# Optimization experiments

Measured on AMD Instinct MI355X. Metric: run time of the kernel, lower is better.

## Reference

```python
import jax, jax.numpy as jnp
import numpy as np

C_IN = 96          # spectral bands
D2 = 2 * C_IN      # d = 192 (inner dim)
D4 = 4 * D2        # 768 (4-directional scan channels)
N = 16             # SSM state size
DR = 6             # delta_rank = ceil(96/16)
B, H, W = 2, 96, 96  # H,W not in {8,16,32,64} -> s=1 path


def setup_inputs() -> dict:
    key = jax.random.key(0)
    ks = jax.random.split(key, 8)
    g = lambda k, shape, s: jax.random.normal(k, shape, jnp.float32) * s
    return {
        "x": jax.random.normal(ks[0], (B, C_IN, H, W), jnp.float32),
        "W_in": g(ks[1], (C_IN, 2 * D2), 0.05),          # in_proj (in,out)
        "b_in": jnp.zeros((2 * D2,), jnp.float32),
        "w_dw": g(ks[2], (D2, 1, 3, 3), 0.1),            # depthwise conv OIHW
        "b_dw": jnp.zeros((D2,), jnp.float32),
        "A_log": jnp.log(jnp.tile(jnp.arange(1.0, N + 1.0, dtype=jnp.float32), (D4, 1))),
        "Dp": jnp.ones((D4,), jnp.float32),
        "W_x": g(ks[3], (D4, DR + 2 * N), 0.05),         # x_proj, no bias
        "W_delta": g(ks[4], (DR, D4), 0.1),
        "b_delta": g(ks[5], (D4,), 0.1),
        "ln_g": jnp.ones((D2,), jnp.float32),
        "ln_b": jnp.zeros((D2,), jnp.float32),
        "W_out": g(ks[6], (D2, C_IN), 0.05),             # out_proj, no bias
    }


def _selective_scan(u, delta, A, Bm, Cm, Dv):
    # u, delta: [b,L,d4]; Bm, Cm: [b,L,n]; A: [d4,n]; Dv: [d4]
    b, L, d4 = u.shape
    n = A.shape[1]

    def step(h, inps):
        u_t, dt, B_t, C_t = inps                      # [b,d4],[b,d4],[b,n],[b,n]
        dA = jnp.exp(dt[:, :, None] * A)              # [b,d4,n]
        h = dA * h + (dt * u_t)[:, :, None] * B_t[:, None, :]
        y = jnp.einsum('bdn,bn->bd', h, C_t) + Dv * u_t
        return h, y

    h0 = jnp.zeros((b, d4, n), u.dtype)
    xs = (jnp.swapaxes(u, 0, 1), jnp.swapaxes(delta, 0, 1),
          jnp.swapaxes(Bm, 0, 1), jnp.swapaxes(Cm, 0, 1))
    _, ys = jax.lax.scan(step, h0, xs)                # ys: [L,b,d4]
    return jnp.swapaxes(ys, 0, 1)                     # [b,L,d4]


def reference(x, W_in, b_in, w_dw, b_dw, A_log, Dp, W_x, W_delta, b_delta, ln_g, ln_b, W_out):
    b, c, Hh, Ww = x.shape                            # s = 1 (H not in {8,16,32,64})
    d = W_in.shape[1] // 2
    # in_proj on channel-last, chunk into x / gate z
    xz = jnp.einsum('bchw,ce->bhwe', x, W_in) + b_in  # [b,h,w,2d]
    xx, z = jnp.split(xz, 2, axis=-1)
    # depthwise conv + silu
    xc = jnp.transpose(xx, (0, 3, 1, 2))              # [b,d,h,w]
    xc = jax.lax.conv_general_dilated(
        xc, w_dw, (1, 1), 'SAME', feature_group_count=d,
        dimension_numbers=('NCHW', 'OIHW', 'NCHW')) + b_dw[None, :, None, None]
    xc = jax.nn.silu(xc)
    # 4 directional flattenings (with s=1: x1==x2 row-major, x3==x4 reversed)
    L = Hh * Ww
    flat = xc.reshape(b, d, L)
    flipped = xc[:, :, ::-1, ::-1].reshape(b, d, L)
    xl = jnp.swapaxes(jnp.concatenate([flat, flat, flipped, flipped], axis=1), 1, 2)  # [b,L,4d]
    # SSM parameterization
    A = -jnp.exp(A_log)                               # [4d,n]
    x_dbl = xl @ W_x                                  # [b,L,dr+2n]
    dr, n = W_delta.shape[0], A.shape[1]
    dt_r = x_dbl[..., :dr]
    Bm = x_dbl[..., dr:dr + n]
    Cm = x_dbl[..., dr + n:]
    delta = jax.nn.softplus(dt_r @ W_delta + b_delta)  # [b,L,4d]
    y = _selective_scan(xl, delta, A, Bm, Cm, Dp)      # [b,L,4d]
    # merge 4 directions back to spatial
    y = jnp.transpose(y.reshape(b, L, 4, d), (0, 2, 3, 1))  # [b,4,d,L]
    y1 = y[:, 0].reshape(b, d, Hh, Ww)
    y2 = y[:, 1].reshape(b, d, Hh, Ww)
    y3 = y[:, 2].reshape(b, d, Hh, Ww)[:, :, ::-1, ::-1]
    y4 = y[:, 3].reshape(b, d, Hh, Ww)[:, :, ::-1, ::-1]
    yh = jnp.transpose(y1 + y2 + y3 + y4, (0, 2, 3, 1))  # [b,h,w,d]
    # LayerNorm over d
    mu = yh.mean(-1, keepdims=True)
    var = ((yh - mu) ** 2).mean(-1, keepdims=True)
    yn = (yh - mu) * jax.lax.rsqrt(var + 1e-5) * ln_g + ln_b
    out = (yn * jax.nn.silu(z)) @ W_out               # [b,h,w,c]
    return jnp.transpose(out, (0, 3, 1, 2))           # [b,c,h,w]
```

## Files before the change

### kernel.cpp

```cpp
#include <hip/hip_runtime.h>
#include <hip/hip_bf16.h>
#include <math.h>

#define CIN 96
#define D2 192
#define D4 768
#define LL 9216
#define NN 16
#define NCH 288
#define CLEN 32

typedef float v2f __attribute__((ext_vector_type(2)));

#define SZ_Y4SLOT (2u*2u*9216u*192u)
#define SZ_BL    (2u*9216u*192u)
#define SZ_XDBL  (2u*9216u*38u)
#define SZ_S     (2u*4u*288u*192u)
#define SZ_HSLOT (2u*4u*288u*192u*8u)
#define F_Y4     0u
#define F_XX     0u
#define F_ZS     (F_Y4 + SZ_Y4SLOT)
#define F_XT     (F_ZS + SZ_BL)
#define F_XD0    (F_XT + SZ_BL)
#define F_XD1    (F_XD0 + SZ_XDBL)
#define F_XD2    (F_XD1 + SZ_XDBL)
#define F_XD3    (F_XD2 + SZ_XDBL)
#define F_SBUF   (F_XD3 + SZ_XDBL)
#define F_HBUF   (F_SBUF + SZ_S)
#define F_WCOMB  (F_HBUF + SZ_HSLOT)
#define F_A0     (F_WCOMB + 15360u)
#define F_FF     (F_A0 + 768u)
#define F_XM     (F_FF + 768u)

__device__ __forceinline__ float silu_f(float z) {
    return z / (1.0f + __expf(-z));
}

__global__ __launch_bounds__(256) void k0_foldw(
    const float* __restrict__ Wx, const float* __restrict__ Alog,
    float* __restrict__ wcomb, float* __restrict__ A0f, float* __restrict__ Ffl)
{
    int i = blockIdx.x * 256 + threadIdx.x;
    if (i < 768) {
        float a0 = -__expf(Alog[i * 16]);
        bool fast = true;
        for (int n = 1; n < 16; n++) {
            float an = -__expf(Alog[i * 16 + n]);
            float tgt = (n + 1) * a0;
            fast = fast && (fabsf(an - tgt) <= 1e-5f * fabsf(tgt));
        }
        A0f[i] = a0;
        Ffl[i] = fast ? 1.f : 0.f;
    }
    if (i >= 192 * 80) return;
    int d = i / 80, j = i % 80;
    float v = 0.f;
    if (j < 38) v = Wx[d * 38 + j] + Wx[(d + 192) * 38 + j];
    else if (j >= 40 && j < 78) {
        int jj = j - 40;
        v = Wx[(d + 384) * 38 + jj] + Wx[(d + 576) * 38 + jj];
    }
    wcomb[i] = v;
}

__global__ __launch_bounds__(256) void k1_inproj(
    const float* __restrict__ x, const float* __restrict__ Win,
    const float* __restrict__ bin, float* __restrict__ xx,
    __hip_bfloat16* __restrict__ zs)
{
    __shared__ float xs[32][68];
    __shared__ float wsh[32][100];
    int tid = threadIdx.x;
    int bid = blockIdx.x;
    int eq = bid & 3;
    int lt = (bid >> 2) % 144;
    int b = bid / 576;
    int l0 = lt * 64;
    int e0 = eq * 96;

    int lg = tid & 15;
    int cg = tid >> 4;
    v2f acc[4][3];
#pragma unroll
    for (int i = 0; i < 4; i++)
#pragma unroll
        for (int p = 0; p < 3; p++) { acc[i][p].x = 0.f; acc[i][p].y = 0.f; }

    for (int kc = 0; kc < 96; kc += 32) {
        __syncthreads();
        for (int i = tid; i < 512; i += 256) {
            int kk = i >> 4, q = i & 15;
            float4 v = *(const float4*)&x[(size_t)(b * 96 + kc + kk) * LL + l0 + q * 4];
            *(float4*)&xs[kk][q * 4] = v;
        }
        for (int i = tid; i < 768; i += 256) {
            int kk = i / 24, q = i - kk * 24;
            float4 v = *(const float4*)&Win[(kc + kk) * 384 + e0 + q * 4];
            *(float4*)&wsh[kk][q * 4] = v;
        }
        __syncthreads();
#pragma unroll 4
        for (int k = 0; k < 32; k++) {
            float4 xv = *(const float4*)&xs[k][lg * 4];
            const v2f* wp = (const v2f*)&wsh[k][cg * 6];
            v2f w0 = wp[0], w1 = wp[1], w2 = wp[2];
            float xa[4] = {xv.x, xv.y, xv.z, xv.w};
#pragma unroll
            for (int i = 0; i < 4; i++) {
                v2f xi; xi.x = xa[i]; xi.y = xa[i];
                acc[i][0] += xi * w0;
                acc[i][1] += xi * w1;
                acc[i][2] += xi * w2;
            }
        }
    }
    if (eq < 2) {
#pragma unroll
        for (int j = 0; j < 6; j++) {
            int e = e0 + cg * 6 + j;
            float bb = bin[e];
            float4 v = {acc[0][j >> 1][j & 1] + bb, acc[1][j >> 1][j & 1] + bb,
                        acc[2][j >> 1][j & 1] + bb, acc[3][j >> 1][j & 1] + bb};
            *(float4*)&xx[(size_t)(b * 192 + e) * LL + l0 + lg * 4] = v;
        }
    } else {
        int zc0 = e0 - 192 + cg * 6;
        float bb[6];
#pragma unroll
        for (int j = 0; j < 6; j++) bb[j] = bin[e0 + cg * 6 + j];
#pragma unroll
        for (int i = 0; i < 4; i++) {
            int l = l0 + lg * 4 + i;
            __hip_bfloat16* zp = &zs[((size_t)b * LL + l) * 192 + zc0];
#pragma unroll
            for (int p = 0; p < 3; p++) {
                __hip_bfloat162 hv = __halves2bfloat162(
                    __float2bfloat16(silu_f(acc[i][p].x + bb[2 * p])),
                    __float2bfloat16(silu_f(acc[i][p].y + bb[2 * p + 1])));
                *(__hip_bfloat162*)&zp[2 * p] = hv;
            }
        }
    }
}

__global__ __launch_bounds__(192) void k2_conv(
    const float* __restrict__ xx, const float* __restrict__ wdw,
    const float* __restrict__ bdw, float* __restrict__ xt)
{
    __shared__ float tile[32][97];
    __shared__ float wsm[32][9];
    __shared__ float bs[32];
    int tid = threadIdx.x;
    int bid = blockIdx.x;
    int h = bid % 96;
    int r = bid / 96;
    int dg = r % 6;
    int b = r / 6;

    for (int i = tid; i < 288; i += 192) wsm[i / 9][i % 9] = wdw[(dg * 32 + i / 9) * 9 + (i % 9)];
    if (tid < 32) bs[tid] = bdw[dg * 32 + tid];
    __syncthreads();

    int w = tid % 96;
    int dhalf = tid / 96;
    for (int p = 0; p < 16; p++) {
        int dsub = 2 * p + dhalf;
        const float* base = xx + (size_t)(b * 192 + dg * 32 + dsub) * LL;
        float acc = bs[dsub];
#pragma unroll
        for (int kh = 0; kh < 3; kh++) {
            int hh = h + kh - 1;
            if (hh < 0 || hh >= 96) continue;
            const float* row = base + hh * 96;
#pragma unroll
            for (int kw = 0; kw < 3; kw++) {
                int ww = w + kw - 1;
                if (ww < 0 || ww >= 96) continue;
                acc += row[ww] * wsm[dsub][kh * 3 + kw];
            }
        }
        tile[dsub][w] = silu_f(acc);
    }
    __syncthreads();
    for (int i = tid; i < 768; i += 192) {
        int q = i & 7, ls = i >> 3;
        float4 v = {tile[q * 4 + 0][ls], tile[q * 4 + 1][ls], tile[q * 4 + 2][ls], tile[q * 4 + 3][ls]};
        *(float4*)&xt[((size_t)b * LL + h * 96 + ls) * 192 + dg * 32 + q * 4] = v;
    }
}

__global__ __launch_bounds__(320) void k3_xdbl(
    const float* __restrict__ xt, const float* __restrict__ wcomb,
    float* __restrict__ xa0, float* __restrict__ xa1,
    float* __restrict__ xb0, float* __restrict__ xb1)
{
    __shared__ float xs[16][68];
    __shared__ float wsh[16][80];
    int tid = threadIdx.x;
    int bid = blockIdx.x;
    int kh = bid & 1;
    int rt = (bid >> 1) % 144;
    int b = bid / 288;
    int r0 = rt * 64;
    int k0 = kh * 96;
    float* __restrict__ xa = kh ? xa1 : xa0;
    float* __restrict__ xb = kh ? xb1 : xb0;

    int rg = tid / 20;
    int cg = tid % 20;
    v2f acc[4][2];
#pragma unroll
    for (int i = 0; i < 4; i++)
#pragma unroll
        for (int p = 0; p < 2; p++) { acc[i][p].x = 0.f; acc[i][p].y = 0.f; }

    for (int kc = 0; kc < 96; kc += 16) {
        __syncthreads();
        if (tid < 256) {
            int row = tid >> 2, dq = tid & 3;
            float4 v = *(const float4*)&xt[((size_t)b * LL + r0 + row) * 192 + k0 + kc + dq * 4];
            xs[dq * 4 + 0][row] = v.x;
            xs[dq * 4 + 1][row] = v.y;
            xs[dq * 4 + 2][row] = v.z;
            xs[dq * 4 + 3][row] = v.w;
        }
        for (int i = tid; i < 16 * 80; i += 320) {
            int d = i / 80, j = i - d * 80;
            wsh[d][j] = wcomb[(k0 + kc + d) * 80 + j];
        }
        __syncthreads();
#pragma unroll
        for (int d = 0; d < 16; d++) {
            float4 xv = *(const float4*)&xs[d][rg * 4];
            float4 wv = *(const float4*)&wsh[d][cg * 4];
            v2f w01; w01.x = wv.x; w01.y = wv.y;
            v2f w23; w23.x = wv.z; w23.y = wv.w;
            float xr[4] = {xv.x, xv.y, xv.z, xv.w};
#pragma unroll
            for (int i = 0; i < 4; i++) {
                v2f xi; xi.x = xr[i]; xi.y = xr[i];
                acc[i][0] += xi * w01;
                acc[i][1] += xi * w23;
            }
        }
    }
    int c0 = cg * 4;
#pragma unroll
    for (int i = 0; i < 4; i++) {
        int la = r0 + rg * 4 + i;
#pragma unroll
        for (int j = 0; j < 4; j++) {
            int col = c0 + j;
            float v = acc[i][j >> 1][j & 1];
            if (col < 38) {
                xa[((size_t)b * LL + la) * 38 + col] = v;
            } else if (col >= 40 && col < 78) {
                int lb = LL - 1 - la;
                xb[((size_t)b * LL + lb) * 38 + (col - 40)] = v;
            }
        }
    }
}

__global__ __launch_bounds__(256) void k3s_merge(
    const float* __restrict__ a0, const float* __restrict__ a1,
    const float* __restrict__ b0, const float* __restrict__ b1,
    float* __restrict__ xm)
{
    int i = blockIdx.x * 256 + threadIdx.x;
    if (i < 2 * LL * 38) xm[i] = (a0[i] + a1[i]) + (b0[i] + b1[i]);
}

__global__ __launch_bounds__(192, 4) void k4_pass1(
    const float* __restrict__ xt, const float* __restrict__ xm,
    const float* __restrict__ Wd, const float* __restrict__ bdl,
    const float* __restrict__ Alog, const float* __restrict__ A0f,
    const float* __restrict__ Ffl,
    float* __restrict__ Sbuf, __hip_bfloat16* __restrict__ Hbuf)
{
    __shared__ float Bt[CLEN][16];
    __shared__ float Dt[CLEN][6];
    int tid = threadIdx.x;
    int bid = blockIdx.x;
    int k = bid % NCH;
    int r = bid / NCH;
    int dir = r & 3;
    int b = r >> 2;
    int l0 = k * CLEN;
    {
        const float* src = xm + ((size_t)b * LL + l0) * 38;
        for (int i = tid; i < CLEN * 38; i += 192) {
            int t = i / 38, j = i - t * 38;
            float v = src[i];
            if (j < 6) Dt[t][j] = v;
            else if (j < 22) Bt[t][j - 6] = v;
        }
    }
    __syncthreads();
    int c = tid;
    int d4 = dir * 192 + c;
    float a0 = A0f[d4];
    bool fast = (Ffl[d4] != 0.f);
    float wd[6];
#pragma unroll
    for (int rr = 0; rr < 6; rr++) wd[rr] = Wd[rr * 768 + d4];
    float bde = bdl[d4];
    float S = 0.f;
    int start = (dir < 2) ? l0 : (LL - 1 - l0);
    ptrdiff_t stp = (dir < 2) ? 192 : -192;
    const float* up = xt + (size_t)b * LL * 192 + (size_t)start * 192 + c;
    int bd = b * 4 + dir;
    size_t base = (((size_t)bd * NCH + k) * 192 + c) * 16;
    if (fast) {
        v2f h2[8];
#pragma unroll
        for (int n = 0; n < 8; n++) { h2[n].x = 0.f; h2[n].y = 0.f; }
#pragma unroll 2
        for (int t = 0; t < CLEN; t++) {
            float2 d01 = *(const float2*)&Dt[t][0];
            float2 d23 = *(const float2*)&Dt[t][2];
            float2 d45 = *(const float2*)&Dt[t][4];
            float s = bde + d01.x * wd[0] + d01.y * wd[1] + d23.x * wd[2]
                          + d23.y * wd[3] + d45.x * wd[4] + d45.y * wd[5];
            float dt = (s > 20.f) ? s : __logf(1.f + __expf(s));
            S += dt;
            float u = *up; up += stp;
            float du = dt * u;
            float e1 = __expf(dt * a0);
            float e2 = e1 * e1;
            v2f q; q.x = e1; q.y = e2;
            v2f e2v; e2v.x = e2; e2v.y = e2;
            v2f e4v = e2v * e2v;
            v2f q2 = q * e2v;
            v2f du2; du2.x = du; du2.y = du;
#pragma unroll
            for (int g = 0; g < 4; g++) {
                float4 bq = *(const float4*)&Bt[t][4 * g];
                v2f b0; b0.x = bq.x; b0.y = bq.y;
                v2f b1; b1.x = bq.z; b1.y = bq.w;
                h2[2 * g]     = q  * h2[2 * g]     + du2 * b0;
                h2[2 * g + 1] = q2 * h2[2 * g + 1] + du2 * b1;
                if (g < 3) { q *= e4v; q2 *= e4v; }
            }
        }
        __hip_bfloat16* hb = Hbuf + base;
#pragma unroll
        for (int n = 0; n < 8; n++) {
            hb[2 * n]     = __float2bfloat16(h2[n].x);
            hb[2 * n + 1] = __float2bfloat16(h2[n].y);
        }
    } else {
        float h[16];
#pragma unroll
        for (int n = 0; n < 16; n++) h[n] = 0.f;
        for (int t = 0; t < CLEN; t++) {
            float s = bde;
#pragma unroll
            for (int rr = 0; rr < 6; rr++) s += Dt[t][rr] * wd[rr];
            float dt = (s > 20.f) ? s : __logf(1.f + __expf(s));
            S += dt;
            float u = *up; up += stp;
            float du = dt * u;
#pragma unroll
            for (int n = 0; n < 16; n++) {
                float e = __expf(dt * (-__expf(Alog[d4 * 16 + n])));
                h[n] = e * h[n] + du * Bt[t][n];
            }
        }
#pragma unroll
        for (int n = 0; n < 16; n++) Hbuf[base + n] = __float2bfloat16(h[n]);
    }
    Sbuf[((size_t)bd * NCH + k) * 192 + c] = S;
}

__global__ __launch_bounds__(256) void k4_pass2(
    const float* __restrict__ Sbuf, const float* __restrict__ Alog,
    __hip_bfloat16* __restrict__ Hbuf)
{
    int lane = blockIdx.x * 256 + threadIdx.x;
    int bd = lane / 3072;
    int cn = lane % 3072;
    int c = cn >> 4, n = cn & 15;
    int dir = bd & 3;
    float an = -__expf(Alog[(dir * 192 + c) * 16 + n]);
    float h = 0.f;
#pragma unroll 8
    for (int k = 0; k < NCH; k++) {
        size_t sidx = ((size_t)bd * NCH + k) * 192 + c;
        float S = Sbuf[sidx];
        size_t idx = sidx * 16 + n;
        float hl = __bfloat162float(Hbuf[idx]);
        float P = __expf(an * S);
        Hbuf[idx] = __float2bfloat16(h);
        h = P * h + hl;
    }
}

__global__ __launch_bounds__(192, 4) void k4_pass3(
    const float* __restrict__ xt, const float* __restrict__ xm,
    const float* __restrict__ Wd, const float* __restrict__ bdl,
    const float* __restrict__ Alog, const float* __restrict__ A0f,
    const float* __restrict__ Ffl, const float* __restrict__ Dp,
    const __hip_bfloat16* __restrict__ Hbuf, __hip_bfloat16* __restrict__ y4)
{
    __shared__ float Bt[CLEN][16];
    __shared__ float Ct[CLEN][16];
    __shared__ float Dt[CLEN][6];
    int tid = threadIdx.x;
    int bid = blockIdx.x;
    int k = bid % NCH;
    int r = bid / NCH;
    int dir = r & 3;
    int b = r >> 2;
    int l0 = k * CLEN;
    {
        const float* src = xm + ((size_t)b * LL + l0) * 38;
        for (int i = tid; i < CLEN * 38; i += 192) {
            int t = i / 38, j = i - t * 38;
            float v = src[i];
            if (j < 6) Dt[t][j] = v;
            else if (j < 22) Bt[t][j - 6] = v;
            else Ct[t][j - 22] = v;
        }
    }
    __syncthreads();
    int c = tid;
    int d4 = dir * 192 + c;
    float a0 = A0f[d4];
    bool fast = (Ffl[d4] != 0.f);
    float wd[6];
#pragma unroll
    for (int rr = 0; rr < 6; rr++) wd[rr] = Wd[rr * 768 + d4];
    float bde = bdl[d4];
    float Dv = Dp[d4];
    int bd = b * 4 + dir;
    size_t base = (((size_t)bd * NCH + k) * 192 + c) * 16;
    int start = (dir < 2) ? l0 : (LL - 1 - l0);
    ptrdiff_t stp = (dir < 2) ? 192 : -192;
    const float* up = xt + (size_t)b * LL * 192 + (size_t)start * 192 + c;
    __hip_bfloat16* yp = y4 + (size_t)bd * LL * 192 + (size_t)start * 192 + c;
    if (fast) {
        v2f h2[8];
        const __hip_bfloat16* hb = Hbuf + base;
#pragma unroll
        for (int n = 0; n < 8; n++) {
            h2[n].x = __bfloat162float(hb[2 * n]);
            h2[n].y = __bfloat162float(hb[2 * n + 1]);
        }
#pragma unroll 2
        for (int t = 0; t < CLEN; t++) {
            float2 d01 = *(const float2*)&Dt[t][0];
            float2 d23 = *(const float2*)&Dt[t][2];
            float2 d45 = *(const float2*)&Dt[t][4];
            float s = bde + d01.x * wd[0] + d01.y * wd[1] + d23.x * wd[2]
                          + d23.y * wd[3] + d45.x * wd[4] + d45.y * wd[5];
            float dt = (s > 20.f) ? s : __logf(1.f + __expf(s));
            float u = *up; up += stp;
            float du = dt * u;
            float e1 = __expf(dt * a0);
            float e2 = e1 * e1;
            v2f q; q.x = e1; q.y = e2;
            v2f e2v; e2v.x = e2; e2v.y = e2;
            v2f e4v = e2v * e2v;
            v2f q2 = q * e2v;
            v2f du2; du2.x = du; du2.y = du;
            v2f ya; ya.x = 0.f; ya.y = 0.f;
            v2f yb; yb.x = 0.f; yb.y = 0.f;
#pragma unroll
            for (int g = 0; g < 4; g++) {
                float4 bq = *(const float4*)&Bt[t][4 * g];
                float4 cq = *(const float4*)&Ct[t][4 * g];
                v2f b0; b0.x = bq.x; b0.y = bq.y;
                v2f b1; b1.x = bq.z; b1.y = bq.w;
                v2f c0v; c0v.x = cq.x; c0v.y = cq.y;
                v2f c1v; c1v.x = cq.z; c1v.y = cq.w;
                h2[2 * g]     = q  * h2[2 * g]     + du2 * b0;
                ya += h2[2 * g] * c0v;
                h2[2 * g + 1] = q2 * h2[2 * g + 1] + du2 * b1;
                yb += h2[2 * g + 1] * c1v;
                if (g < 3) { q *= e4v; q2 *= e4v; }
            }
            float yv = (ya.x + ya.y) + (yb.x + yb.y) + Dv * u;
            *yp = __float2bfloat16(yv); yp += stp;
        }
    } else {
        float h[16];
#pragma unroll
        for (int n = 0; n < 16; n++) h[n] = __bfloat162float(Hbuf[base + n]);
        for (int t = 0; t < CLEN; t++) {
            float s = bde;
#pragma unroll
            for (int rr = 0; rr < 6; rr++) s += Dt[t][rr] * wd[rr];
            float dt = (s > 20.f) ? s : __logf(1.f + __expf(s));
            float u = *up; up += stp;
            float du = dt * u;
            float yv = Dv * u;
#pragma unroll
            for (int n = 0; n < 16; n++) {
                float e = __expf(dt * (-__expf(Alog[d4 * 16 + n])));
                h[n] = e * h[n] + du * Bt[t][n];
                yv += h[n] * Ct[t][n];
            }
            *yp = __float2bfloat16(yv); yp += stp;
        }
    }
}

__global__ __launch_bounds__(256) void k5_out(
    const __hip_bfloat16* __restrict__ y4, const __hip_bfloat16* __restrict__ zs,
    const float* __restrict__ lng, const float* __restrict__ lnb,
    const float* __restrict__ Wout, float* __restrict__ out)
{
    __shared__ float acts[16][196];
    __shared__ float wsh[32][100];
    int tid = threadIdx.x;
    int wv = tid >> 6;
    int lane = tid & 63;
    int gl0 = blockIdx.x * 16;
    int b = gl0 / LL;
    int l0 = gl0 % LL;
    const size_t ds = (size_t)LL * 192;

    for (int i = 0; i < 4; i++) {
        int rrow = wv * 4 + i;
        int l = l0 + rrow;
        float yv[3], zv[3];
        float s1 = 0.f, s2 = 0.f;
#pragma unroll
        for (int kk = 0; kk < 3; kk++) {
            int c = lane + kk * 64;
            size_t off = ((size_t)(b * 4) * LL + l) * 192 + c;
            float y = __bfloat162float(y4[off]) + __bfloat162float(y4[off + ds])
                    + __bfloat162float(y4[off + 2 * ds]) + __bfloat162float(y4[off + 3 * ds]);
            yv[kk] = y;
            zv[kk] = __bfloat162float(zs[((size_t)b * LL + l) * 192 + c]);
            s1 += y; s2 += y * y;
        }
#pragma unroll
        for (int o = 32; o; o >>= 1) {
            s1 += __shfl_xor(s1, o, 64);
            s2 += __shfl_xor(s2, o, 64);
        }
        float mean = s1 * (1.f / 192.f);
        float var = s2 * (1.f / 192.f) - mean * mean;
        float rs = rsqrtf(var + 1e-5f);
#pragma unroll
        for (int kk = 0; kk < 3; kk++) {
            int c = lane + kk * 64;
            float yn = (yv[kk] - mean) * rs * lng[c] + lnb[c];
            acts[rrow][c] = yn * zv[kk];
        }
    }

    int ty = tid & 15;
    int tx = tid >> 4;
    v2f o2[3];
    o2[0].x = 0.f; o2[0].y = 0.f;
    o2[1].x = 0.f; o2[1].y = 0.f;
    o2[2].x = 0.f; o2[2].y = 0.f;

    for (int kc = 0; kc < 192; kc += 32) {
        __syncthreads();
        for (int i = tid; i < 32 * 24; i += 256) {
            int d = i / 24, q = i - d * 24;
            *(float4*)&wsh[d][q * 4] = *(const float4*)&Wout[(kc + d) * 96 + q * 4];
        }
        __syncthreads();
#pragma unroll
        for (int kk = 0; kk < 32; kk++) {
            float av = acts[ty][kc + kk];
            const v2f* wp = (const v2f*)&wsh[kk][tx * 6];
            v2f w0 = wp[0], w1 = wp[1], w2 = wp[2];
            v2f sp; sp.x = av; sp.y = av;
            o2[0] += sp * w0;
            o2[1] += sp * w1;
            o2[2] += sp * w2;
        }
    }
    int l = l0 + ty;
#pragma unroll
    for (int j = 0; j < 6; j++) {
        int n = tx * 6 + j;
        out[((size_t)(b * 96) + n) * LL + l] = o2[j >> 1][j & 1];
    }
}

extern "C" void kernel_launch(void* const* d_in, const int* in_sizes, int n_in,
                              void* d_out, int out_size, void* d_ws, size_t ws_size,
                              hipStream_t stream)
{
    const float* x    = (const float*)d_in[0];
    const float* Win  = (const float*)d_in[1];
    const float* bin  = (const float*)d_in[2];
    const float* wdw  = (const float*)d_in[3];
    const float* bdw  = (const float*)d_in[4];
    const float* Alog = (const float*)d_in[5];
    const float* Dp   = (const float*)d_in[6];
    const float* Wx   = (const float*)d_in[7];
    const float* Wd   = (const float*)d_in[8];
    const float* bdl  = (const float*)d_in[9];
    const float* lng  = (const float*)d_in[10];
    const float* lnb  = (const float*)d_in[11];
    const float* Wout = (const float*)d_in[12];
    float* out = (float*)d_out;

    float* ws    = (float*)d_ws;
    __hip_bfloat16* y4 = (__hip_bfloat16*)(ws + F_Y4);
    float* xx    = ws + F_XX;
    __hip_bfloat16* zs = (__hip_bfloat16*)(ws + F_ZS);
    float* xt    = ws + F_XT;
    float* xd0   = ws + F_XD0;
    float* xd1   = ws + F_XD1;
    float* xd2   = ws + F_XD2;
    float* xd3   = ws + F_XD3;
    float* Sbuf  = ws + F_SBUF;
    __hip_bfloat16* Hbuf = (__hip_bfloat16*)(ws + F_HBUF);
    float* wcomb = ws + F_WCOMB;
    float* A0f   = ws + F_A0;
    float* Ffl   = ws + F_FF;
    float* xm    = ws + F_XM;

    k0_foldw<<<60, 256, 0, stream>>>(Wx, Alog, wcomb, A0f, Ffl);
    k1_inproj<<<1152, 256, 0, stream>>>(x, Win, bin, xx, zs);
    k2_conv<<<1152, 192, 0, stream>>>(xx, wdw, bdw, xt);
    k3_xdbl<<<576, 320, 0, stream>>>(xt, wcomb, xd0, xd1, xd2, xd3);
    k3s_merge<<<2736, 256, 0, stream>>>(xd0, xd1, xd2, xd3, xm);
    k4_pass1<<<2304, 192, 0, stream>>>(xt, xm, Wd, bdl, Alog, A0f, Ffl, Sbuf, Hbuf);
    k4_pass2<<<96, 256, 0, stream>>>(Sbuf, Alog, Hbuf);
    k4_pass3<<<2304, 192, 0, stream>>>(xt, xm, Wd, bdl, Alog, A0f, Ffl, Dp, Hbuf, y4);
    k5_out<<<1152, 256, 0, stream>>>(y4, zs, lng, lnb, Wout, out);
}
```

Measured before the change: 289.1 us.

## Fuse x_dbl partial-sum merge into projection kernel and vectorize output loads

The x_dbl projection kernel now computes the full 192-deep reduction per 32-row tile. It loads both the forward rows and the mirrored reversed rows, and combines the forward and flipped halves through shared memory before a single store to xm. This removes four partial buffers and the separate merge kernel launch. k4_pass1 now reads only the 22 used columns of xm, and k5_out loads bf16 pairs instead of scalars. In exchange each block does twice the K loop, and half its threads idle during the staging loads.

```diff
diff --git a/kernel.cpp b/kernel.cpp
--- a/kernel.cpp
+++ b/kernel.cpp
@@ -21,16 +21,12 @@
 #define F_XX     0u
 #define F_ZS     (F_Y4 + SZ_Y4SLOT)
 #define F_XT     (F_ZS + SZ_BL)
-#define F_XD0    (F_XT + SZ_BL)
-#define F_XD1    (F_XD0 + SZ_XDBL)
-#define F_XD2    (F_XD1 + SZ_XDBL)
-#define F_XD3    (F_XD2 + SZ_XDBL)
-#define F_SBUF   (F_XD3 + SZ_XDBL)
+#define F_XM     (F_XT + SZ_BL)
+#define F_SBUF   (F_XM + SZ_XDBL)
 #define F_HBUF   (F_SBUF + SZ_S)
 #define F_WCOMB  (F_HBUF + SZ_HSLOT)
 #define F_A0     (F_WCOMB + 15360u)
 #define F_FF     (F_A0 + 768u)
-#define F_XM     (F_FF + 768u)
 
 __device__ __forceinline__ float silu_f(float z) {
     return z / (1.0f + __expf(-z));
@@ -191,84 +187,86 @@
 
 __global__ __launch_bounds__(320) void k3_xdbl(
     const float* __restrict__ xt, const float* __restrict__ wcomb,
-    float* __restrict__ xa0, float* __restrict__ xa1,
-    float* __restrict__ xb0, float* __restrict__ xb1)
-{
-    __shared__ float xs[16][68];
+    float* __restrict__ xm)
+{
+    __shared__ float xsf[16][36];
+    __shared__ float xsr[16][36];
     __shared__ float wsh[16][80];
+    __shared__ float rtile[32][40];
     int tid = threadIdx.x;
     int bid = blockIdx.x;
-    int kh = bid & 1;
-    int rt = (bid >> 1) % 144;
+    int rt = bid % 288;
     int b = bid / 288;
-    int r0 = rt * 64;
-    int k0 = kh * 96;
-    float* __restrict__ xa = kh ? xa1 : xa0;
-    float* __restrict__ xb = kh ? xb1 : xb0;
+    int r0 = rt * 32;
 
     int rg = tid / 20;
     int cg = tid % 20;
-    v2f acc[4][2];
-#pragma unroll
-    for (int i = 0; i < 4; i++)
+    bool isf = (cg < 10);
+    v2f acc[2][2];
+#pragma unroll
+    for (int i = 0; i < 2; i++)
 #pragma unroll
         for (int p = 0; p < 2; p++) { acc[i][p].x = 0.f; acc[i][p].y = 0.f; }
 
-    for (int kc = 0; kc < 96; kc += 16) {
+    for (int kc = 0; kc < 192; kc += 16) {
         __syncthreads();
-        if (tid < 256) {
-            int row = tid >> 2, dq = tid & 3;
-            float4 v = *(const float4*)&xt[((size_t)b * LL + r0 + row) * 192 + k0 + kc + dq * 4];
-            xs[dq * 4 + 0][row] = v.x;
-            xs[dq * 4 + 1][row] = v.y;
-            xs[dq * 4 + 2][row] = v.z;
-            xs[dq * 4 + 3][row] = v.w;
-        }
-        for (int i = tid; i < 16 * 80; i += 320) {
-            int d = i / 80, j = i - d * 80;
-            wsh[d][j] = wcomb[(k0 + kc + d) * 80 + j];
+        if (tid < 128) {
+            int row = tid >> 2, q = tid & 3;
+            float4 v = *(const float4*)&xt[((size_t)b * LL + r0 + row) * 192 + kc + q * 4];
+            xsf[q * 4 + 0][row] = v.x;
+            xsf[q * 4 + 1][row] = v.y;
+            xsf[q * 4 + 2][row] = v.z;
+            xsf[q * 4 + 3][row] = v.w;
+        } else if (tid < 256) {
+            int row = (tid - 128) >> 2, q = tid & 3;
+            float4 v = *(const float4*)&xt[((size_t)b * LL + (LL - 1 - r0 - row)) * 192 + kc + q * 4];
+            xsr[q * 4 + 0][row] = v.x;
+            xsr[q * 4 + 1][row] = v.y;
+            xsr[q * 4 + 2][row] = v.z;
+            xsr[q * 4 + 3][row] = v.w;
+        }
+        for (int i = tid; i < 1280; i += 320) {
+            wsh[i / 80][i - (i / 80) * 80] = wcomb[(kc + i / 80) * 80 + (i - (i / 80) * 80)];
         }
         __syncthreads();
+        const float (*xs)[36] = isf ? xsf : xsr;
 #pragma unroll
         for (int d = 0; d < 16; d++) {
-            float4 xv = *(const float4*)&xs[d][rg * 4];
+            float2 xv = *(const float2*)&xs[d][rg * 2];
             float4 wv = *(const float4*)&wsh[d][cg * 4];
             v2f w01; w01.x = wv.x; w01.y = wv.y;
             v2f w23; w23.x = wv.z; w23.y = wv.w;
-            float xr[4] = {xv.x, xv.y, xv.z, xv.w};
-#pragma unroll
-            for (int i = 0; i < 4; i++) {
-                v2f xi; xi.x = xr[i]; xi.y = xr[i];
-                acc[i][0] += xi * w01;
-                acc[i][1] += xi * w23;
-            }
+            v2f x0; x0.x = xv.x; x0.y = xv.x;
+            v2f x1; x1.x = xv.y; x1.y = xv.y;
+            acc[0][0] += x0 * w01;
+            acc[0][1] += x0 * w23;
+            acc[1][0] += x1 * w01;
+            acc[1][1] += x1 * w23;
         }
     }
     int c0 = cg * 4;
-#pragma unroll
-    for (int i = 0; i < 4; i++) {
-        int la = r0 + rg * 4 + i;
-#pragma unroll
-        for (int j = 0; j < 4; j++) {
-            int col = c0 + j;
-            float v = acc[i][j >> 1][j & 1];
-            if (col < 38) {
-                xa[((size_t)b * LL + la) * 38 + col] = v;
-            } else if (col >= 40 && col < 78) {
-                int lb = LL - 1 - la;
-                xb[((size_t)b * LL + lb) * 38 + (col - 40)] = v;
-            }
-        }
-    }
-}
-
-__global__ __launch_bounds__(256) void k3s_merge(
-    const float* __restrict__ a0, const float* __restrict__ a1,
-    const float* __restrict__ b0, const float* __restrict__ b1,
-    float* __restrict__ xm)
-{
-    int i = blockIdx.x * 256 + threadIdx.x;
-    if (i < 2 * LL * 38) xm[i] = (a0[i] + a1[i]) + (b0[i] + b1[i]);
+    if (!isf) {
+#pragma unroll
+        for (int i = 0; i < 2; i++)
+#pragma unroll
+            for (int j = 0; j < 4; j++)
+                rtile[rg * 2 + i][c0 - 40 + j] = acc[i][j >> 1][j & 1];
+    }
+    __syncthreads();
+    if (isf) {
+#pragma unroll
+        for (int i = 0; i < 2; i++) {
+            int la = r0 + rg * 2 + i;
+#pragma unroll
+            for (int j = 0; j < 4; j++) {
+                int col = c0 + j;
+                if (col < 38) {
+                    float v = acc[i][j >> 1][j & 1] + rtile[rg * 2 + i][col];
+                    xm[((size_t)b * LL + la) * 38 + col] = v;
+                }
+            }
+        }
+    }
 }
 
 __global__ __launch_bounds__(192, 4) void k4_pass1(
@@ -289,11 +287,11 @@
     int l0 = k * CLEN;
     {
         const float* src = xm + ((size_t)b * LL + l0) * 38;
-        for (int i = tid; i < CLEN * 38; i += 192) {
-            int t = i / 38, j = i - t * 38;
-            float v = src[i];
+        for (int i = tid; i < CLEN * 22; i += 192) {
+            int t = i / 22, j = i - t * 22;
+            float v = src[t * 38 + j];
             if (j < 6) Dt[t][j] = v;
-            else if (j < 22) Bt[t][j - 6] = v;
+            else Bt[t][j - 6] = v;
         }
     }
     __syncthreads();
@@ -524,17 +522,32 @@
     for (int i = 0; i < 4; i++) {
         int rrow = wv * 4 + i;
         int l = l0 + rrow;
-        float yv[3], zv[3];
+        float ypr[2][2], zpr[2][2];
         float s1 = 0.f, s2 = 0.f;
 #pragma unroll
-        for (int kk = 0; kk < 3; kk++) {
-            int c = lane + kk * 64;
-            size_t off = ((size_t)(b * 4) * LL + l) * 192 + c;
-            float y = __bfloat162float(y4[off]) + __bfloat162float(y4[off + ds])
-                    + __bfloat162float(y4[off + 2 * ds]) + __bfloat162float(y4[off + 3 * ds]);
-            yv[kk] = y;
-            zv[kk] = __bfloat162float(zs[((size_t)b * LL + l) * 192 + c]);
-            s1 += y; s2 += y * y;
+        for (int kk = 0; kk < 2; kk++) {
+            int pair = kk * 64 + lane;
+            bool act = (kk == 0) || (lane < 32);
+            float y0 = 0.f, y1 = 0.f, z0 = 0.f, z1 = 0.f;
+            if (act) {
+                int cbase = pair * 2;
+                size_t off = ((size_t)(b * 4) * LL + l) * 192 + cbase;
+                __hip_bfloat162 v0 = *(const __hip_bfloat162*)&y4[off];
+                __hip_bfloat162 v1 = *(const __hip_bfloat162*)&y4[off + ds];
+                __hip_bfloat162 v2 = *(const __hip_bfloat162*)&y4[off + 2 * ds];
+                __hip_bfloat162 v3 = *(const __hip_bfloat162*)&y4[off + 3 * ds];
+                y0 = __bfloat162float(v0.x) + __bfloat162float(v1.x)
+                   + __bfloat162float(v2.x) + __bfloat162float(v3.x);
+                y1 = __bfloat162float(v0.y) + __bfloat162float(v1.y)
+                   + __bfloat162float(v2.y) + __bfloat162float(v3.y);
+                __hip_bfloat162 zv = *(const __hip_bfloat162*)&zs[((size_t)b * LL + l) * 192 + cbase];
+                z0 = __bfloat162float(zv.x);
+                z1 = __bfloat162float(zv.y);
+                s1 += y0 + y1;
+                s2 += y0 * y0 + y1 * y1;
+            }
+            ypr[kk][0] = y0; ypr[kk][1] = y1;
+            zpr[kk][0] = z0; zpr[kk][1] = z1;
         }
 #pragma unroll
         for (int o = 32; o; o >>= 1) {
@@ -545,10 +558,17 @@
         float var = s2 * (1.f / 192.f) - mean * mean;
         float rs = rsqrtf(var + 1e-5f);
 #pragma unroll
-        for (int kk = 0; kk < 3; kk++) {
-            int c = lane + kk * 64;
-            float yn = (yv[kk] - mean) * rs * lng[c] + lnb[c];
-            acts[rrow][c] = yn * zv[kk];
+        for (int kk = 0; kk < 2; kk++) {
+            bool act = (kk == 0) || (lane < 32);
+            if (act) {
+                int cbase = (kk * 64 + lane) * 2;
+#pragma unroll
+                for (int p = 0; p < 2; p++) {
+                    int cc = cbase + p;
+                    float yn = (ypr[kk][p] - mean) * rs * lng[cc] + lnb[cc];
+                    acts[rrow][cc] = yn * zpr[kk][p];
+                }
+            }
         }
     }
 
@@ -609,22 +629,17 @@
     float* xx    = ws + F_XX;
     __hip_bfloat16* zs = (__hip_bfloat16*)(ws + F_ZS);
     float* xt    = ws + F_XT;
-    float* xd0   = ws + F_XD0;
-    float* xd1   = ws + F_XD1;
-    float* xd2   = ws + F_XD2;
-    float* xd3   = ws + F_XD3;
+    float* xm    = ws + F_XM;
     float* Sbuf  = ws + F_SBUF;
     __hip_bfloat16* Hbuf = (__hip_bfloat16*)(ws + F_HBUF);
     float* wcomb = ws + F_WCOMB;
     float* A0f   = ws + F_A0;
     float* Ffl   = ws + F_FF;
-    float* xm    = ws + F_XM;
 
     k0_foldw<<<60, 256, 0, stream>>>(Wx, Alog, wcomb, A0f, Ffl);
     k1_inproj<<<1152, 256, 0, stream>>>(x, Win, bin, xx, zs);
     k2_conv<<<1152, 192, 0, stream>>>(xx, wdw, bdw, xt);
-    k3_xdbl<<<576, 320, 0, stream>>>(xt, wcomb, xd0, xd1, xd2, xd3);
-    k3s_merge<<<2736, 256, 0, stream>>>(xd0, xd1, xd2, xd3, xm);
+    k3_xdbl<<<576, 320, 0, stream>>>(xt, wcomb, xm);
     k4_pass1<<<2304, 192, 0, stream>>>(xt, xm, Wd, bdl, Alog, A0f, Ffl, Sbuf, Hbuf);
     k4_pass2<<<96, 256, 0, stream>>>(Sbuf, Alog, Hbuf);
     k4_pass3<<<2304, 192, 0, stream>>>(xt, xm, Wd, bdl, Alog, A0f, Ffl, Dp, Hbuf, y4);
```

New measurement: 293.2 us. About the same (+1.4%).
